# Kernel tuning notes

Measured on AMD Instinct MI355X. Metric: run time of the kernel, lower is better.

The kernel has to match this reference:

```python
import jax, jax.numpy as jnp
import numpy as np
import math

B, N, T, D, H, NOUT = 32, 20, 100, 4, 128, 16
E = N * (N - 1)
EPS = 1e-5

def _conv1d(x, w, b):
    # x: [M, Cin, L], w: [Cout, Cin, K] -> [M, Cout, L-K+1] (VALID, stride 1)
    y = jax.lax.conv_general_dilated(x, w, (1,), 'VALID', dimension_numbers=('NCH', 'OIH', 'NCH'))
    return y + b[None, :, None]

def _bn(x, g, b, axes, caxis):
    # training-mode batch norm (biased variance), eps as in torch
    m = jnp.mean(x, axis=axes, keepdims=True)
    v = jnp.var(x, axis=axes, keepdims=True)
    sh = [1] * x.ndim
    sh[caxis] = -1
    return (x - m) / jnp.sqrt(v + EPS) * g.reshape(sh) + b.reshape(sh)

def _mlp(x, w1, b1, w2, b2, g, bb):
    h = jax.nn.elu(x @ w1.T + b1)
    h = jax.nn.elu(h @ w2.T + b2)
    return _bn(h, g, bb, (0, 1), 2)  # BN over B*E samples per feature

def _forward(rel_rec, rel_send, inputs, conv1_w, conv1_b, bn1_g, bn1_b, conv2_w, conv2_b, bn2_g, bn2_b, pred_w, pred_b, att_w, att_b, mlp1_w1, mlp1_b1, mlp1_w2, mlp1_b2, mlp1_g, mlp1_bb, mlp2_w1, mlp2_b1, mlp2_w2, mlp2_b2, mlp2_g, mlp2_bb, mlp3_w1, mlp3_b1, mlp3_w2, mlp3_b2, mlp3_g, mlp3_bb, fc_out_w, fc_out_b):
    Bv, Nv, Tv, Dv = inputs.shape
    Ev = Nv * (Nv - 1)
    # node2edge_temporal: gather sender/receiver trajectories -> [B*E, 2D, T]
    xf = inputs.reshape(Bv, Nv, Tv * Dv)
    recv = jnp.einsum('en,bnf->bef', rel_rec, xf).reshape(Bv * Ev, Tv, Dv).transpose(0, 2, 1)
    send = jnp.einsum('en,bnf->bef', rel_send, xf).reshape(Bv * Ev, Tv, Dv).transpose(0, 2, 1)
    edges = jnp.concatenate([send, recv], axis=1)
    # CNN over time
    h = jax.nn.relu(_conv1d(edges, conv1_w, conv1_b))
    h = _bn(h, bn1_g, bn1_b, (0, 2), 1)
    L = h.shape[-1] // 2
    h = h[:, :, : 2 * L].reshape(h.shape[0], h.shape[1], L, 2).max(axis=-1)  # maxpool k=2 s=2
    h = jax.nn.relu(_conv1d(h, conv2_w, conv2_b))
    h = _bn(h, bn2_g, bn2_b, (0, 2), 1)
    pred = jnp.einsum('bct,oc->bot', h, pred_w[:, :, 0]) + pred_b[None, :, None]
    att = jax.nn.softmax(jnp.einsum('bct,oc->bot', h, att_w[:, :, 0]) + att_b[None, :, None], axis=-1)
    x = (pred * att).mean(axis=-1).reshape(Bv, Ev, -1)  # attention-weighted mean pool
    x = _mlp(x, mlp1_w1, mlp1_b1, mlp1_w2, mlp1_b2, mlp1_g, mlp1_bb)
    x_skip = x
    # edge2node: scatter-mean into receivers (divide by N)
    xn = jnp.einsum('en,beh->bnh', rel_rec, x) / Nv
    xn = _mlp(xn, mlp2_w1, mlp2_b1, mlp2_w2, mlp2_b2, mlp2_g, mlp2_bb)
    # node2edge: gather back to edges
    es = jnp.einsum('en,bnh->beh', rel_send, xn)
    er = jnp.einsum('en,bnh->beh', rel_rec, xn)
    x = jnp.concatenate([es, er, x_skip], axis=2)
    x = _mlp(x, mlp3_w1, mlp3_b1, mlp3_w2, mlp3_b2, mlp3_g, mlp3_bb)
    return x @ fc_out_w.T + fc_out_b

def setup_inputs() -> dict:
    key = jax.random.key(0)
    ks = iter(jax.random.split(key, 64))
    def rn(shape, scale):
        return jax.random.normal(next(ks), shape, dtype=jnp.float32) * scale
    def xav(fo, fi):
        return rn((fo, fi), math.sqrt(2.0 / (fo + fi)))
    inputs = rn((B, N, T, D), 1.0)
    pairs = np.array([(i, j) for i in range(N) for j in range(N) if i != j])
    eye = np.eye(N, dtype=np.float32)
    d = {'inputs': inputs,
         'rel_rec': jnp.asarray(eye[pairs[:, 0]]),
         'rel_send': jnp.asarray(eye[pairs[:, 1]])}
    d['conv1_w'] = rn((H, 2 * D, 5), math.sqrt(2.0 / (5 * H)))
    d['conv1_b'] = jnp.full((H,), 0.1, jnp.float32)
    d['bn1_g'] = jnp.ones((H,), jnp.float32); d['bn1_b'] = jnp.zeros((H,), jnp.float32)
    d['conv2_w'] = rn((H, H, 5), math.sqrt(2.0 / (5 * H)))
    d['conv2_b'] = jnp.full((H,), 0.1, jnp.float32)
    d['bn2_g'] = jnp.ones((H,), jnp.float32); d['bn2_b'] = jnp.zeros((H,), jnp.float32)
    d['pred_w'] = rn((H, H, 1), math.sqrt(2.0 / H))
    d['pred_b'] = jnp.full((H,), 0.1, jnp.float32)
    d['att_w'] = rn((1, H, 1), math.sqrt(2.0))
    d['att_b'] = jnp.full((1,), 0.1, jnp.float32)
    for nm, fi in (('mlp1', H), ('mlp2', H), ('mlp3', 3 * H)):
        d[nm + '_w1'] = xav(H, fi); d[nm + '_b1'] = jnp.full((H,), 0.1, jnp.float32)
        d[nm + '_w2'] = xav(H, H); d[nm + '_b2'] = jnp.full((H,), 0.1, jnp.float32)
        d[nm + '_g'] = jnp.ones((H,), jnp.float32); d[nm + '_bb'] = jnp.zeros((H,), jnp.float32)
    d['fc_out_w'] = xav(NOUT, H)
    d['fc_out_b'] = jnp.full((NOUT,), 0.1, jnp.float32)
    return d

def reference(inputs, rel_rec, rel_send, conv1_w, conv1_b, bn1_g, bn1_b, conv2_w, conv2_b, bn2_g, bn2_b, pred_w, pred_b, att_w, att_b, mlp1_w1, mlp1_b1, mlp1_w2, mlp1_b2, mlp1_g, mlp1_bb, mlp2_w1, mlp2_b1, mlp2_w2, mlp2_b2, mlp2_g, mlp2_bb, mlp3_w1, mlp3_b1, mlp3_w2, mlp3_b2, mlp3_g, mlp3_bb, fc_out_w, fc_out_b):
    return _forward(rel_rec, rel_send, inputs, conv1_w, conv1_b, bn1_g, bn1_b, conv2_w, conv2_b, bn2_g, bn2_b, pred_w, pred_b, att_w, att_b, mlp1_w1, mlp1_b1, mlp1_w2, mlp1_b2, mlp1_g, mlp1_bb, mlp2_w1, mlp2_b1, mlp2_w2, mlp2_b2, mlp2_g, mlp2_bb, mlp3_w1, mlp3_b1, mlp3_w2, mlp3_b2, mlp3_g, mlp3_bb, fc_out_w, fc_out_b)
```

## Files before the change

### kernel.cpp

```cpp
#include <hip/hip_runtime.h>
#include <hip/hip_bf16.h>
#include <hip/hip_fp16.h>

#define BB 32
#define NN 20
#define TT 100
#define DD 4
#define HH 128
#define EE 380
#define BE 12160
#define L1 96
#define LP 48
#define L2 44
#define NOUT 16
#define EPS 1e-5f
#define NREP 64

typedef _Float16 f16x8 __attribute__((ext_vector_type(8)));
typedef _Float16 f16x4 __attribute__((ext_vector_type(4)));
typedef _Float16 f16x2 __attribute__((ext_vector_type(2)));
typedef float f32x4 __attribute__((ext_vector_type(4)));

#define S_BIAS2 0
#define S_BN1_SC 256
#define S_BN2_SC 768

#define OFF_STATS 0ULL
#define OFF_SIDX 16384ULL
#define OFF_RIDX 18432ULL
#define OFF_INC 20480ULL
#define OFF_Y23 24576ULL
#define OFF_X 149446656ULL
#define OFF_BUFA 155672576ULL
#define OFF_BUFB 161898496ULL
#define OFF_XN 168124416ULL
#define OFF_T640 168452096ULL
#define OFF_REPM 168779776ULL
#define OFF_MP 171958272ULL
#define OFF_APACK OFF_T640
#define OFF_APACK1 (OFF_T640 + 163840ULL)
#define OFF_PWT (OFF_T640 + 180224ULL)
#define OFF_W2SUM (OFF_T640 + 245760ULL)
#define OFF_REP1 OFF_BUFA
#define OFF_REP2 (OFF_BUFA + 65536ULL)
#define MP_M1W1 0
#define MP_M1W2 16384
#define MP_M2W1 32768
#define MP_M2W2 49152
#define MP_M3W2 65536
#define MP_M3W1 81920

__device__ __forceinline__ float eluf(float v) { return v > 0.f ? v : expm1f(v); }

__global__ __launch_bounds__(256) void k_prep(const float* __restrict__ rel_rec,
                                              const float* __restrict__ rel_send,
                                              const float* __restrict__ w2,
                                              const float* __restrict__ w1,
                                              const float* __restrict__ pred_w,
                                              const float* __restrict__ m1w1,
                                              const float* __restrict__ m1w2,
                                              const float* __restrict__ m2w1,
                                              const float* __restrict__ m2w2,
                                              const float* __restrict__ m3w1,
                                              const float* __restrict__ m3w2,
                                              _Float16* __restrict__ apack,
                                              _Float16* __restrict__ apack1,
                                              float* __restrict__ pwt,
                                              float* __restrict__ w2sum,
                                              _Float16* __restrict__ mp,
                                              float* rep1, float* rep2, float* repm,
                                              int* sidx, int* ridx, int* inc) {
    int b = blockIdx.x;
    int tid = threadIdx.x;
    int l = tid & 63;
    if (b < 40) {
        int f = b * 4 + (tid >> 6);
        int m0 = f & 7, ks = f >> 3, s = ks & 3, k = ks >> 2;
        int m = m0 * 16 + (l & 15);
        int cbase = 32 * s + (l >> 4) * 8;
#pragma unroll
        for (int j = 0; j < 8; ++j)
            apack[(f * 64 + l) * 8 + j] = (_Float16)w2[m * 640 + (cbase + j) * 5 + k];
    } else if (b < 44) {
        int f = (b - 40) * 4 + (tid >> 6);
        int m0 = f & 7, s = f >> 3;
        int m = m0 * 16 + (l & 15);
        int cbase = 32 * s + (l >> 4) * 8;
#pragma unroll
        for (int j = 0; j < 8; ++j) {
            int c = cbase + j;
            int k = c >> 3, ci = c & 7;
            apack1[(f * 64 + l) * 8 + j] = (k < 5) ? (_Float16)w1[m * 40 + ci * 5 + k]
                                                   : (_Float16)0.f;
        }
    } else if (b == 44) {
        for (int i = tid; i < NREP * 256; i += 256) { rep1[i] = 0.f; rep2[i] = 0.f; }
        for (int i = tid; i < 3 * NREP * 256; i += 256) repm[i] = 0.f;
        for (int e = tid; e < EE; e += 256) {
            int s = 0, r = 0;
            for (int n = 0; n < NN; ++n) {
                if (rel_send[e * NN + n] > 0.5f) s = n;
                if (rel_rec[e * NN + n] > 0.5f) r = n;
            }
            sidx[e] = s; ridx[e] = r;
        }
        __syncthreads();
        if (tid < NN) {
            int k = 0;
// ... 91 lines not shown
                    s_y2t[(t >> 1) * 136 + co0 + r] = (_Float16)fmaxf(v, p);
            }
        }
#pragma unroll
        for (int r = 0; r < 4; ++r) {
            float s = ss[r], q = qq[r];
            s += __shfl_xor(s, 1); s += __shfl_xor(s, 2); s += __shfl_xor(s, 4); s += __shfl_xor(s, 8);
            q += __shfl_xor(q, 1); q += __shfl_xor(q, 2); q += __shfl_xor(q, 4); q += __shfl_xor(q, 8);
            if (l15 == 0) {
                atomicAdd(&rep[co0 + r], s);
                atomicAdd(&rep[128 + co0 + r], q);
            }
        }
    }
    __syncthreads();
    _Float16* dst = y2p + (long long)be * 6144;
    for (int chunk = threadIdx.x; chunk < 768; chunk += 256) {
        int row = chunk >> 4, off = (chunk & 15) * 8;
        *(f16x8*)(dst + row * 128 + off) = *(const f16x8*)(&s_y2t[row * 136 + off]);
    }
}

__global__ void k_finalize_rep(float* __restrict__ rep, float* stats, int scIdx,
                               const float* __restrict__ g, const float* __restrict__ bb,
                               float inv_count) {
    int j = threadIdx.x;
    float s = 0.f, q = 0.f;
    for (int i = 0; i < NREP; ++i) {
        s += rep[i * 256 + j];
        q += rep[i * 256 + 128 + j];
    }
    for (int i = 0; i < NREP; ++i) {
        rep[i * 256 + j] = 0.f;
        rep[i * 256 + 128 + j] = 0.f;
    }
    float m = s * inv_count;
    float v = fmaxf(q * inv_count - m * m, 0.f);
    float sc = g[j] * rsqrtf(v + EPS);
    stats[scIdx + j] = sc;
    stats[scIdx + 128 + j] = bb[j] - m * sc;
}

__global__ void k_finalize_bn1(float* __restrict__ rep, float* stats,
                               const float* __restrict__ g, const float* __restrict__ bb,
                               const float* __restrict__ w2sum, const float* __restrict__ conv2_b,
                               float inv_count) {
    __shared__ float s_sh[128];
    int j = threadIdx.x;
    float s = 0.f, q = 0.f;
    for (int i = 0; i < NREP; ++i) {
        s += rep[i * 256 + j];
        q += rep[i * 256 + 128 + j];
    }
    for (int i = 0; i < NREP; ++i) {
        rep[i * 256 + j] = 0.f;
        rep[i * 256 + 128 + j] = 0.f;
    }
    float m = s * inv_count;
    float v = fmaxf(q * inv_count - m * m, 0.f);
    float sc = g[j] * rsqrtf(v + EPS);
    float sh = bb[j] - m * sc;
    stats[S_BN1_SC + j] = sc;
    stats[S_BN1_SC + 128 + j] = sh;
    s_sh[j] = sh;
    __syncthreads();
    float acc = conv2_b[j];
    for (int ci = 0; ci < 128; ++ci)
        acc = fmaf(w2sum[j * 128 + ci], s_sh[ci], acc);
    stats[S_BIAS2 + j] = acc;
}

__global__ __launch_bounds__(256) void k_scale(_Float16* __restrict__ apack,
                                               const float* __restrict__ stats) {
    int tid = threadIdx.x, l = tid & 63;
    int f = blockIdx.x * 4 + (tid >> 6);
    int s = (f >> 3) & 3;
    int cbase = 32 * s + (l >> 4) * 8;
    _Float16* p = apack + (f * 64 + l) * 8;
#pragma unroll
    for (int j = 0; j < 8; ++j)
        p[j] = (_Float16)((float)p[j] * stats[S_BN1_SC + cbase + j]);
}

__global__ __launch_bounds__(256) void k_conv2(_Float16* __restrict__ y23,
                                               const _Float16* __restrict__ apack,
                                               const float* __restrict__ stats,
                                               float* rep2) {
    __shared__ __align__(16) _Float16 s_y2t[2][48 * 136];
    int tid = threadIdx.x;
    int be0 = blockIdx.x * 2;
    for (int i = tid; i < 1536; i += 256) {
        int ed = i / 768, rem = i - ed * 768;
        int row = rem >> 4, c0 = (rem & 15) * 8;
        *(f16x8*)(&s_y2t[ed][row * 136 + c0]) =
            *(const f16x8*)(y23 + (long long)(be0 + ed) * 6144 + rem * 8);
    }
    __syncthreads();
    int w = tid >> 6, lane = tid & 63;
    int quad = lane >> 4, l15 = lane & 15;
    int g = w & 1, e = w >> 1;
    f32x4 acc[4][3];
#pragma unroll
    for (int m = 0; m < 4; ++m)
#pragma unroll
        for (int nt = 0; nt < 3; ++nt) acc[m][nt] = (f32x4){0.f, 0.f, 0.f, 0.f};
    const f16x8* Ap = (const f16x8*)apack;
    const char* base = (const char*)&s_y2t[e][0];
#pragma unroll
    for (int k = 0; k < 5; ++k) {
#pragma unroll
        for (int s = 0; s < 4; ++s) {
            f16x8 am[4];
#pragma unroll
            for (int m = 0; m < 4; ++m)
                am[m] = Ap[((k * 4 + s) * 8 + g * 4 + m) * 64 + lane];
#pragma unroll
            for (int nt = 0; nt < 3; ++nt) {
                int r = nt * 16 + l15 + k;
                if (nt == 2) r = (r > 47) ? 47 : r;
                f16x8 bfr = *(const f16x8*)(base + r * 272 + 64 * s + quad * 16);
#pragma unroll
                for (int m = 0; m < 4; ++m)
                    acc[m][nt] = __builtin_amdgcn_mfma_f32_16x16x32_f16(am[m], bfr, acc[m][nt], 0, 0, 0);
            }
        }
    }
    int be = be0 + e;
    _Float16* y3 = y23 + (long long)be * 6144;
    float* rep = rep2 + (be & (NREP - 1)) * 256;
#pragma unroll
    for (int m = 0; m < 4; ++m) {
        int co0 = (g * 4 + m) * 16 + quad * 4;
        float4 bs = *(const float4*)(stats + S_BIAS2 + co0);
        float ssum[4] = {0.f, 0.f, 0.f, 0.f}, qsum[4] = {0.f, 0.f, 0.f, 0.f};
#pragma unroll
        for (int nt = 0; nt < 3; ++nt) {
            int t = nt * 16 + l15;
            if (t < 44) {
                float v0 = fmaxf(acc[m][nt][0] + bs.x, 0.f);
                float v1 = fmaxf(acc[m][nt][1] + bs.y, 0.f);
                float v2 = fmaxf(acc[m][nt][2] + bs.z, 0.f);
                float v3 = fmaxf(acc[m][nt][3] + bs.w, 0.f);
                f16x4 o = {(_Float16)v0, (_Float16)v1, (_Float16)v2, (_Float16)v3};
                *(f16x4*)(y3 + t * 128 + co0) = o;
                ssum[0] += v0; qsum[0] += v0 * v0;
                ssum[1] += v1; qsum[1] += v1 * v1;
                ssum[2] += v2; qsum[2] += v2 * v2;
                ssum[3] += v3; qsum[3] += v3 * v3;
            }
        }
#pragma unroll
        for (int r = 0; r < 4; ++r) {
            float s = ssum[r], q = qsum[r];
            s += __shfl_xor(s, 1); s += __shfl_xor(s, 2); s += __shfl_xor(s, 4); s += __shfl_xor(s, 8);
            q += __shfl_xor(q, 1); q += __shfl_xor(q, 2); q += __shfl_xor(q, 4); q += __shfl_xor(q, 8);
            if (l15 == 0) {
                atomicAdd(&rep[co0 + r], s);
                atomicAdd(&rep[128 + co0 + r], q);
            }
        }
    }
}

__global__ __launch_bounds__(256) void k_predatt(const _Float16* __restrict__ y23,
                                                 const float* __restrict__ stats,
                                                 const float* __restrict__ att_w,
                                                 const float* __restrict__ att_b,
                                                 const float* __restrict__ pwt,
                                                 const float* __restrict__ pred_b,
                                                 float* __restrict__ x) {
    __shared__ float h[44 * 132];
    __shared__ float s_att[48];
    __shared__ float s_p1[256];
    __shared__ float s_p2[256];
    __shared__ float s_sc[128], s_sh[128];
    int be = blockIdx.x, tid = threadIdx.x;
    if (tid < 128) {
        s_sc[tid] = stats[S_BN2_SC + tid];
        s_sh[tid] = stats[S_BN2_SC + 128 + tid];
    }
    __syncthreads();
    const _Float16* yp = y23 + (long long)be * 6144;
    for (int i = tid; i < 704; i += 256) {
        int t = i >> 4, c0 = (i & 15) * 8;
        f16x8 v = *(const f16x8*)(yp + i * 8);
        float4 a, bq;
        a.x = fmaf((float)v[0], s_sc[c0 + 0], s_sh[c0 + 0]);
        a.y = fmaf((float)v[1], s_sc[c0 + 1], s_sh[c0 + 1]);
        a.z = fmaf((float)v[2], s_sc[c0 + 2], s_sh[c0 + 2]);
        a.w = fmaf((float)v[3], s_sc[c0 + 3], s_sh[c0 + 3]);
        bq.x = fmaf((float)v[4], s_sc[c0 + 4], s_sh[c0 + 4]);
        bq.y = fmaf((float)v[5], s_sc[c0 + 5], s_sh[c0 + 5]);
        bq.z = fmaf((float)v[6], s_sc[c0 + 6], s_sh[c0 + 6]);
        bq.w = fmaf((float)v[7], s_sc[c0 + 7], s_sh[c0 + 7]);
        *(float4*)(&h[t * 132 + c0]) = a;
        *(float4*)(&h[t * 132 + c0 + 4]) = bq;
    }
    __syncthreads();
    int w = tid >> 6, lane = tid & 63;
    {
        float aw0 = att_w[lane], aw1 = att_w[64 + lane];
        for (int tt = 0; tt < 11; ++tt) {
            int t = w * 11 + tt;
            float p = h[t * 132 + lane] * aw0 + h[t * 132 + 64 + lane] * aw1;
            p += __shfl_xor(p, 1); p += __shfl_xor(p, 2); p += __shfl_xor(p, 4);
            p += __shfl_xor(p, 8); p += __shfl_xor(p, 16); p += __shfl_xor(p, 32);
            if (lane == 0) s_att[t] = p + att_b[0];
        }
    }
    __syncthreads();
    if (w == 0) {
        float v = (lane < 44) ? s_att[lane] : -1e30f;
        float m = v;
        m = fmaxf(m, __shfl_xor(m, 1)); m = fmaxf(m, __shfl_xor(m, 2));
        m = fmaxf(m, __shfl_xor(m, 4)); m = fmaxf(m, __shfl_xor(m, 8));
        m = fmaxf(m, __shfl_xor(m, 16)); m = fmaxf(m, __shfl_xor(m, 32));
        float ev = (lane < 44) ? expf(v - m) : 0.f;
        float ss = ev;
        ss += __shfl_xor(ss, 1); ss += __shfl_xor(ss, 2); ss += __shfl_xor(ss, 4);
        ss += __shfl_xor(ss, 8); ss += __shfl_xor(ss, 16); ss += __shfl_xor(ss, 32);
        if (lane < 44) s_att[lane] = ev / ss;
    }
    __syncthreads();
    {
        int c = tid & 127, hh = tid >> 7;
        float a = 0.f;
        for (int t = hh * 22; t < hh * 22 + 22; ++t) a = fmaf(h[t * 132 + c], s_att[t], a);
        s_p1[tid] = a;
    }
    __syncthreads();
    {
        int o = tid & 127, hh = tid >> 7;
        float a = 0.f;
        for (int c = hh * 64; c < hh * 64 + 64; ++c) {
            float hw = s_p1[c] + s_p1[128 + c];
            a = fmaf(pwt[c * 128 + o], hw, a);
        }
        s_p2[tid] = a;
    }
    __syncthreads();
    if (tid < 128) {
        float a = s_p2[tid] + s_p2[128 + tid] + pred_b[tid];
        x[(long long)be * 128 + tid] = a * (1.0f / 44.0f);
    }
}

__global__ __launch_bounds__(256) void k_mlp2x(const float* __restrict__ in,
                                               const _Float16* __restrict__ wp1,
                                               const float* __restrict__ b1,
                                               const _Float16* __restrict__ wp2,
                                               const float* __restrict__ b2,
                                               float* __restrict__ out,
                                               float* __restrict__ repm) {
    __shared__ __align__(16) _Float16 s_in[64 * 136];
    __shared__ __align__(16) _Float16 s_mid[64 * 136];
    int tid = threadIdx.x;
    long long r0 = (long long)blockIdx.x * 64;
    {
        const float4* src = (const float4*)(in + r0 * 128);
        for (int i = tid; i < 2048; i += 256) {
            int row = i >> 5, c0 = (i & 31) * 4;
            float4 v = src[i];
            f16x4 o = {(_Float16)v.x, (_Float16)v.y, (_Float16)v.z, (_Float16)v.w};
            *(f16x4*)(&s_in[row * 136 + c0]) = o;
        }
    }
    __syncthreads();
    int w = tid >> 6, lane = tid & 63, quad = lane >> 4, l15 = lane & 15;
    {
        f32x4 acc[2][4];
#pragma unroll
        for (int m = 0; m < 2; ++m)
#pragma unroll
            for (int nt = 0; nt < 4; ++nt) acc[m][nt] = (f32x4){0.f, 0.f, 0.f, 0.f};
        const f16x8* Ap = (const f16x8*)wp1;
#pragma unroll
        for (int s = 0; s < 4; ++s) {
            f16x8 a0 = Ap[(s * 8 + 2 * w) * 64 + lane];
            f16x8 a1 = Ap[(s * 8 + 2 * w + 1) * 64 + lane];
#pragma unroll
            for (int nt = 0; nt < 4; ++nt) {
                f16x8 bfr = *(const f16x8*)((const char*)s_in + (nt * 16 + l15) * 272 + 64 * s + quad * 16);
                acc[0][nt] = __builtin_amdgcn_mfma_f32_16x16x32_f16(a0, bfr, acc[0][nt], 0, 0, 0);
                acc[1][nt] = __builtin_amdgcn_mfma_f32_16x16x32_f16(a1, bfr, acc[1][nt], 0, 0, 0);
            }
        }
#pragma unroll
        for (int m = 0; m < 2; ++m) {
            int j0 = (2 * w + m) * 16 + quad * 4;
            float4 bs = *(const float4*)(b1 + j0);
#pragma unroll
            for (int nt = 0; nt < 4; ++nt) {
                int row = nt * 16 + l15;
                f16x4 o = {(_Float16)eluf(acc[m][nt][0] + bs.x),
                           (_Float16)eluf(acc[m][nt][1] + bs.y),
                           (_Float16)eluf(acc[m][nt][2] + bs.z),
                           (_Float16)eluf(acc[m][nt][3] + bs.w)};
                *(f16x4*)(&s_mid[row * 136 + j0]) = o;
            }
        }
    }
    __syncthreads();
    {
        f32x4 acc[2][4];
#pragma unroll
        for (int m = 0; m < 2; ++m)
#pragma unroll
            for (int nt = 0; nt < 4; ++nt) acc[m][nt] = (f32x4){0.f, 0.f, 0.f, 0.f};
        const f16x8* Ap = (const f16x8*)wp2;
#pragma unroll
        for (int s = 0; s < 4; ++s) {
            f16x8 a0 = Ap[(s * 8 + 2 * w) * 64 + lane];
            f16x8 a1 = Ap[(s * 8 + 2 * w + 1) * 64 + lane];
#pragma unroll
            for (int nt = 0; nt < 4; ++nt) {
                f16x8 bfr = *(const f16x8*)((const char*)s_mid + (nt * 16 + l15) * 272 + 64 * s + quad * 16);
                acc[0][nt] = __builtin_amdgcn_mfma_f32_16x16x32_f16(a0, bfr, acc[0][nt], 0, 0, 0);
                acc[1][nt] = __builtin_amdgcn_mfma_f32_16x16x32_f16(a1, bfr, acc[1][nt], 0, 0, 0);
            }
        }
#pragma unroll
        for (int m = 0; m < 2; ++m) {
            int j0 = (2 * w + m) * 16 + quad * 4;
            float4 bs = *(const float4*)(b2 + j0);
            float ss[4] = {0.f, 0.f, 0.f, 0.f}, qq[4] = {0.f, 0.f, 0.f, 0.f};
#pragma unroll
// ... 207 lines not shown
    __shared__ float s_w[16 * 129];
    __shared__ float s_sc[128], s_sh[128];
    int r0 = blockIdx.x * 16;
    int tid = threadIdx.x;
    if (tid < 128) {
        float s = 0.f, q = 0.f;
        for (int i = 0; i < NREP; ++i) {
            s += repm3[i * 256 + tid];
            q += repm3[i * 256 + 128 + tid];
        }
        float mm = s * (1.0f / (float)BE);
        float vv = fmaxf(q * (1.0f / (float)BE) - mm * mm, 0.f);
        float sc = m3g[tid] * rsqrtf(vv + EPS);
        s_sc[tid] = sc;
        s_sh[tid] = m3bb[tid] - mm * sc;
    }
    __syncthreads();
    for (int i = tid; i < 16 * 128; i += 256) {
        int rr = i >> 7, j = i & 127;
        s_x[rr * 129 + j] = fmaf(h2[(long long)(r0 + rr) * 128 + j], s_sc[j], s_sh[j]);
    }
    for (int i = tid; i < 16 * 128; i += 256) {
        int o = i >> 7, j = i & 127;
        s_w[o * 129 + j] = fcw[i];
    }
    __syncthreads();
    int rl = tid >> 4, o = tid & 15;
    float a = fcb[o];
    for (int j = 0; j < 128; ++j) a = fmaf(s_x[rl * 129 + j], s_w[o * 129 + j], a);
    out[(long long)(r0 + rl) * 16 + o] = a;
}

extern "C" void kernel_launch(void* const* d_in, const int* in_sizes, int n_in,
                              void* d_out, int out_size, void* d_ws, size_t ws_size,
                              hipStream_t stream) {
    const float* inputs = (const float*)d_in[0];
    const float* rel_rec = (const float*)d_in[1];
    const float* rel_send = (const float*)d_in[2];
    const float* conv1_w = (const float*)d_in[3];
    const float* conv1_b = (const float*)d_in[4];
    const float* bn1_g = (const float*)d_in[5];
    const float* bn1_b = (const float*)d_in[6];
    const float* conv2_w = (const float*)d_in[7];
    const float* conv2_b = (const float*)d_in[8];
    const float* bn2_g = (const float*)d_in[9];
    const float* bn2_b = (const float*)d_in[10];
    const float* pred_w = (const float*)d_in[11];
    const float* pred_b = (const float*)d_in[12];
    const float* att_w = (const float*)d_in[13];
    const float* att_b = (const float*)d_in[14];
    const float* m1w1 = (const float*)d_in[15];
    const float* m1b1 = (const float*)d_in[16];
    const float* m1w2 = (const float*)d_in[17];
    const float* m1b2 = (const float*)d_in[18];
    const float* m1g = (const float*)d_in[19];
    const float* m1bb = (const float*)d_in[20];
    const float* m2w1 = (const float*)d_in[21];
    const float* m2b1 = (const float*)d_in[22];
    const float* m2w2 = (const float*)d_in[23];
    const float* m2b2 = (const float*)d_in[24];
    const float* m2g = (const float*)d_in[25];
    const float* m2bb = (const float*)d_in[26];
    const float* m3w1 = (const float*)d_in[27];
    const float* m3b1 = (const float*)d_in[28];
    const float* m3w2 = (const float*)d_in[29];
    const float* m3b2 = (const float*)d_in[30];
    const float* m3g = (const float*)d_in[31];
    const float* m3bb = (const float*)d_in[32];
    const float* fcw = (const float*)d_in[33];
    const float* fcb = (const float*)d_in[34];

    char* ws = (char*)d_ws;
    float* stats = (float*)(ws + OFF_STATS);
    int* sidx = (int*)(ws + OFF_SIDX);
    int* ridx = (int*)(ws + OFF_RIDX);
    int* inc = (int*)(ws + OFF_INC);
    _Float16* y23 = (_Float16*)(ws + OFF_Y23);
    float* x = (float*)(ws + OFF_X);
    float* bufB = (float*)(ws + OFF_BUFB);
    float* xn = (float*)(ws + OFF_XN);
    _Float16* apack = (_Float16*)(ws + OFF_APACK);
    _Float16* apack1 = (_Float16*)(ws + OFF_APACK1);
    float* pwt = (float*)(ws + OFF_PWT);
    float* w2sum = (float*)(ws + OFF_W2SUM);
    float* rep1 = (float*)(ws + OFF_REP1);
    float* rep2 = (float*)(ws + OFF_REP2);
    float* repm1 = (float*)(ws + OFF_REPM);
    float* repm2 = (float*)(ws + OFF_REPM + 65536ULL);
    float* repm3 = (float*)(ws + OFF_REPM + 131072ULL);
    _Float16* mp = (_Float16*)(ws + OFF_MP);
    float* outp = (float*)d_out;

    hipLaunchKernelGGL(k_prep, dim3(125), dim3(256), 0, stream,
                       rel_rec, rel_send, conv2_w, conv1_w, pred_w,
                       m1w1, m1w2, m2w1, m2w2, m3w1, m3w2,
                       apack, apack1, pwt, w2sum, mp, rep1, rep2, repm1, sidx, ridx, inc);
    hipLaunchKernelGGL(k_conv1_stats, dim3(BE), dim3(256), 0, stream,
                       inputs, apack1, conv1_b, sidx, ridx, rep1, y23);
    hipLaunchKernelGGL(k_finalize_bn1, dim3(1), dim3(128), 0, stream,
                       rep1, stats, bn1_g, bn1_b, w2sum, conv2_b, 1.0f / (float)(BE * L1));
    hipLaunchKernelGGL(k_scale, dim3(40), dim3(256), 0, stream, apack, stats);
    hipLaunchKernelGGL(k_conv2, dim3(BE / 2), dim3(256), 0, stream,
                       y23, apack, stats, rep2);
    hipLaunchKernelGGL(k_finalize_rep, dim3(1), dim3(128), 0, stream,
                       rep2, stats, S_BN2_SC, bn2_g, bn2_b, 1.0f / (float)(BE * L2));
    hipLaunchKernelGGL(k_predatt, dim3(BE), dim3(256), 0, stream,
                       y23, stats, att_w, att_b, pwt, pred_b, x);
    hipLaunchKernelGGL(k_mlp2x, dim3(BE / 64), dim3(256), 0, stream,
                       x, mp + MP_M1W1, m1b1, mp + MP_M1W2, m1b2, bufB, repm1);
    hipLaunchKernelGGL(k_e2n, dim3(BB * NN), dim3(128), 0, stream, bufB, inc, repm1, m1g, m1bb, xn);
    hipLaunchKernelGGL(k_mlp2x, dim3(BB * NN / 64), dim3(256), 0, stream,
                       xn, mp + MP_M2W1, m2b1, mp + MP_M2W2, m2b2, xn, repm2);
    hipLaunchKernelGGL(k_mlp3x, dim3(BE / 64), dim3(256), 0, stream,
                       xn, bufB, sidx, ridx, repm1, repm2, m1g, m1bb, m2g, m2bb,
                       mp + MP_M3W1, m3b1, mp + MP_M3W2, m3b2, bufB, repm3);
    hipLaunchKernelGGL(k_fcout, dim3(BE / 16), dim3(256), 0, stream,
                       bufB, repm3, m3g, m3bb, fcw, fcb, outp);
    (void)in_sizes; (void)n_in; (void)out_size; (void)ws_size;
}
```

Baseline: 587.0 us.

## Process four edges per conv2 block with A-fragment reuse and staged coalesced stores

The conv2 kernel now handles four edge sequences per block, and each wave computes two edges so every loaded weight fragment feeds twice as many MFMAs. Weight fragments are double-buffered across the K/S loop to overlap their global loads with compute. Outputs are written into shared memory first and then copied out with coalesced 16-byte stores instead of scattered 8-byte stores. The cost is double the accumulator registers (launch_bounds with 2 blocks/SM), double the shared memory, and half as many blocks.

```diff
diff --git a/kernel.cpp b/kernel.cpp
--- a/kernel.cpp
+++ b/kernel.cpp
@@ -281,84 +281,124 @@
         p[j] = (_Float16)((float)p[j] * stats[S_BN1_SC + cbase + j]);
 }
 
-__global__ __launch_bounds__(256) void k_conv2(_Float16* __restrict__ y23,
-                                               const _Float16* __restrict__ apack,
-                                               const float* __restrict__ stats,
-                                               float* rep2) {
-    __shared__ __align__(16) _Float16 s_y2t[2][48 * 136];
+#define C2_COMPUTE(AM, K, S)                                                          \
+    do {                                                                              \
+        int rbase = ((K) * 272) + ((S) * 64) + lquad16 + l15x272;                     \
+        _Pragma("unroll")                                                             \
+        for (int nt = 0; nt < 3; ++nt) {                                              \
+            int ro = rbase + nt * (16 * 272);                                         \
+            if (nt == 2) { int rr = 32 + l15 + (K); if (rr > 47) ro -= (rr - 47) * 272; } \
+            f16x8 b0 = *(const f16x8*)(baseE0 + ro);                                  \
+            f16x8 b1 = *(const f16x8*)(baseE1 + ro);                                  \
+            _Pragma("unroll")                                                         \
+            for (int m = 0; m < 4; ++m) {                                             \
+                acc0[m][nt] = __builtin_amdgcn_mfma_f32_16x16x32_f16(AM[m], b0, acc0[m][nt], 0, 0, 0); \
+                acc1[m][nt] = __builtin_amdgcn_mfma_f32_16x16x32_f16(AM[m], b1, acc1[m][nt], 0, 0, 0); \
+            }                                                                         \
+        }                                                                             \
+    } while (0)
+
+#define C2_EPILOG(ACC, EE)                                                            \
+    do {                                                                              \
+        int e_loc = ep * 2 + (EE);                                                    \
+        long long bee = be0 + e_loc;                                                  \
+        float* rep = rep2 + ((int)(bee & (NREP - 1))) * 256;                          \
+        _Float16* sout = &s_y2t[e_loc][0];                                            \
+        _Pragma("unroll")                                                             \
+        for (int m = 0; m < 4; ++m) {                                                 \
+            int co0 = (g * 4 + m) * 16 + quad * 4;                                    \
+            float4 bs = *(const float4*)(stats + S_BIAS2 + co0);                      \
+            float ssum[4] = {0.f, 0.f, 0.f, 0.f}, qsum[4] = {0.f, 0.f, 0.f, 0.f};     \
+            _Pragma("unroll")                                                         \
+            for (int nt = 0; nt < 3; ++nt) {                                          \
+                int t = nt * 16 + l15;                                                \
+                if (t < 44) {                                                         \
+                    float v0 = fmaxf(ACC[m][nt][0] + bs.x, 0.f);                      \
+                    float v1 = fmaxf(ACC[m][nt][1] + bs.y, 0.f);                      \
+                    float v2 = fmaxf(ACC[m][nt][2] + bs.z, 0.f);                      \
+                    float v3 = fmaxf(ACC[m][nt][3] + bs.w, 0.f);                      \
+                    f16x4 o = {(_Float16)v0, (_Float16)v1, (_Float16)v2, (_Float16)v3}; \
+                    *(f16x4*)(sout + t * 136 + co0) = o;                              \
+                    ssum[0] += v0; qsum[0] += v0 * v0;                                \
+                    ssum[1] += v1; qsum[1] += v1 * v1;                                \
+                    ssum[2] += v2; qsum[2] += v2 * v2;                                \
+                    ssum[3] += v3; qsum[3] += v3 * v3;                                \
+                }                                                                     \
+            }                                                                         \
+            _Pragma("unroll")                                                         \
+            for (int r = 0; r < 4; ++r) {                                             \
+                float s = ssum[r], q = qsum[r];                                       \
+                s += __shfl_xor(s, 1); s += __shfl_xor(s, 2); s += __shfl_xor(s, 4); s += __shfl_xor(s, 8); \
+                q += __shfl_xor(q, 1); q += __shfl_xor(q, 2); q += __shfl_xor(q, 4); q += __shfl_xor(q, 8); \
+                if (l15 == 0) {                                                       \
+                    atomicAdd(&rep[co0 + r], s);                                      \
+                    atomicAdd(&rep[128 + co0 + r], q);                                \
+                }                                                                     \
+            }                                                                         \
+        }                                                                             \
+    } while (0)
+
+__global__ __launch_bounds__(256, 2) void k_conv2(_Float16* __restrict__ y23,
+                                                  const _Float16* __restrict__ apack,
+                                                  const float* __restrict__ stats,
+                                                  float* rep2) {
+    __shared__ __align__(16) _Float16 s_y2t[4][48 * 136];
     int tid = threadIdx.x;
-    int be0 = blockIdx.x * 2;
-    for (int i = tid; i < 1536; i += 256) {
-        int ed = i / 768, rem = i - ed * 768;
-        int row = rem >> 4, c0 = (rem & 15) * 8;
-        *(f16x8*)(&s_y2t[ed][row * 136 + c0]) =
-            *(const f16x8*)(y23 + (long long)(be0 + ed) * 6144 + rem * 8);
-    }
+    long long be0 = (long long)blockIdx.x * 4;
+#pragma unroll
+    for (int ed = 0; ed < 4; ++ed)
+        for (int rem = tid; rem < 768; rem += 256) {
+            int row = rem >> 4, c0 = (rem & 15) * 8;
+            *(f16x8*)(&s_y2t[ed][row * 136 + c0]) =
+                *(const f16x8*)(y23 + (be0 + ed) * 6144 + rem * 8);
+        }
     __syncthreads();
     int w = tid >> 6, lane = tid & 63;
     int quad = lane >> 4, l15 = lane & 15;
-    int g = w & 1, e = w >> 1;
-    f32x4 acc[4][3];
+    int g = w & 1, ep = w >> 1;
+    int lquad16 = quad * 16;
+    int l15x272 = l15 * 272;
+    const char* baseE0 = (const char*)&s_y2t[ep * 2][0];
+    const char* baseE1 = (const char*)&s_y2t[ep * 2 + 1][0];
+    f32x4 acc0[4][3], acc1[4][3];
 #pragma unroll
     for (int m = 0; m < 4; ++m)
 #pragma unroll
-        for (int nt = 0; nt < 3; ++nt) acc[m][nt] = (f32x4){0.f, 0.f, 0.f, 0.f};
+        for (int nt = 0; nt < 3; ++nt) {
+            acc0[m][nt] = (f32x4){0.f, 0.f, 0.f, 0.f};
+            acc1[m][nt] = (f32x4){0.f, 0.f, 0.f, 0.f};
+        }
     const f16x8* Ap = (const f16x8*)apack;
-    const char* base = (const char*)&s_y2t[e][0];
-#pragma unroll
-    for (int k = 0; k < 5; ++k) {
-#pragma unroll
-        for (int s = 0; s < 4; ++s) {
-            f16x8 am[4];
-#pragma unroll
-            for (int m = 0; m < 4; ++m)
-                am[m] = Ap[((k * 4 + s) * 8 + g * 4 + m) * 64 + lane];
-#pragma unroll
-            for (int nt = 0; nt < 3; ++nt) {
-                int r = nt * 16 + l15 + k;
-                if (nt == 2) r = (r > 47) ? 47 : r;
-                f16x8 bfr = *(const f16x8*)(base + r * 272 + 64 * s + quad * 16);
-#pragma unroll
-                for (int m = 0; m < 4; ++m)
-                    acc[m][nt] = __builtin_amdgcn_mfma_f32_16x16x32_f16(am[m], bfr, acc[m][nt], 0, 0, 0);
-            }
-        }
-    }
-    int be = be0 + e;
-    _Float16* y3 = y23 + (long long)be * 6144;
-    float* rep = rep2 + (be & (NREP - 1)) * 256;
-#pragma unroll
-    for (int m = 0; m < 4; ++m) {
-        int co0 = (g * 4 + m) * 16 + quad * 4;
-        float4 bs = *(const float4*)(stats + S_BIAS2 + co0);
-        float ssum[4] = {0.f, 0.f, 0.f, 0.f}, qsum[4] = {0.f, 0.f, 0.f, 0.f};
-#pragma unroll
-        for (int nt = 0; nt < 3; ++nt) {
-            int t = nt * 16 + l15;
-            if (t < 44) {
-                float v0 = fmaxf(acc[m][nt][0] + bs.x, 0.f);
-                float v1 = fmaxf(acc[m][nt][1] + bs.y, 0.f);
-                float v2 = fmaxf(acc[m][nt][2] + bs.z, 0.f);
-                float v3 = fmaxf(acc[m][nt][3] + bs.w, 0.f);
-                f16x4 o = {(_Float16)v0, (_Float16)v1, (_Float16)v2, (_Float16)v3};
-                *(f16x4*)(y3 + t * 128 + co0) = o;
-                ssum[0] += v0; qsum[0] += v0 * v0;
-                ssum[1] += v1; qsum[1] += v1 * v1;
-                ssum[2] += v2; qsum[2] += v2 * v2;
-                ssum[3] += v3; qsum[3] += v3 * v3;
-            }
-        }
-#pragma unroll
-        for (int r = 0; r < 4; ++r) {
-            float s = ssum[r], q = qsum[r];
-            s += __shfl_xor(s, 1); s += __shfl_xor(s, 2); s += __shfl_xor(s, 4); s += __shfl_xor(s, 8);
-            q += __shfl_xor(q, 1); q += __shfl_xor(q, 2); q += __shfl_xor(q, 4); q += __shfl_xor(q, 8);
-            if (l15 == 0) {
-                atomicAdd(&rep[co0 + r], s);
-                atomicAdd(&rep[128 + co0 + r], q);
-            }
-        }
-    }
+    f16x8 amA[4], amB[4];
+#pragma unroll
+    for (int m = 0; m < 4; ++m) amA[m] = Ap[(g * 4 + m) * 64 + lane];
+    for (int it = 0; it < 20; it += 2) {
+#pragma unroll
+        for (int m = 0; m < 4; ++m) amB[m] = Ap[((it + 1) * 8 + g * 4 + m) * 64 + lane];
+        {
+            int k = it >> 2, s = it & 3;
+            C2_COMPUTE(amA, k, s);
+        }
+        if (it + 2 < 20) {
+#pragma unroll
+            for (int m = 0; m < 4; ++m) amA[m] = Ap[((it + 2) * 8 + g * 4 + m) * 64 + lane];
+        }
+        {
+            int k = (it + 1) >> 2, s = (it + 1) & 3;
+            C2_COMPUTE(amB, k, s);
+        }
+    }
+    __syncthreads();
+    C2_EPILOG(acc0, 0);
+    C2_EPILOG(acc1, 1);
+    __syncthreads();
+#pragma unroll
+    for (int ed = 0; ed < 4; ++ed)
+        for (int rem = tid; rem < 704; rem += 256) {
+            int row = rem >> 4, c0 = (rem & 15) * 8;
+            *(f16x8*)(y23 + (be0 + ed) * 6144 + rem * 8) =
+                *(const f16x8*)(&s_y2t[ed][row * 136 + c0]);
+        }
 }
 
 __global__ __launch_bounds__(256) void k_predatt(const _Float16* __restrict__ y23,
@@ -832,7 +872,7 @@
     hipLaunchKernelGGL(k_finalize_bn1, dim3(1), dim3(128), 0, stream,
                        rep1, stats, bn1_g, bn1_b, w2sum, conv2_b, 1.0f / (float)(BE * L1));
     hipLaunchKernelGGL(k_scale, dim3(40), dim3(256), 0, stream, apack, stats);
-    hipLaunchKernelGGL(k_conv2, dim3(BE / 2), dim3(256), 0, stream,
+    hipLaunchKernelGGL(k_conv2, dim3(BE / 4), dim3(256), 0, stream,
                        y23, apack, stats, rep2);
     hipLaunchKernelGGL(k_finalize_rep, dim3(1), dim3(128), 0, stream,
                        rep2, stats, S_BN2_SC, bn2_g, bn2_b, 1.0f / (float)(BE * L2));
```

Result: slower. 606.8 us (+3.4%).

## Split conv2 across 8 waves with two output tiles each and double-buffered A loads

Applied to the files above, without the earlier changes.

The conv2 kernel goes from 256 to 512 threads per block, so each wave computes 2 instead of 4 output-channel tiles. This cuts accumulator registers per wave and raises occupancy, with launch bounds allowing 6 blocks. The A-fragment loads are software-pipelined with two register buffers so the next k-step's weights load while the current MFMAs run. The cost is that each B fragment read from LDS now feeds only 2 MFMAs instead of 4, so LDS read traffic per MFMA roughly doubles.

```diff
diff --git a/kernel.cpp b/kernel.cpp
--- a/kernel.cpp
+++ b/kernel.cpp
@@ -281,55 +281,63 @@
         p[j] = (_Float16)((float)p[j] * stats[S_BN1_SC + cbase + j]);
 }
 
-__global__ __launch_bounds__(256) void k_conv2(_Float16* __restrict__ y23,
-                                               const _Float16* __restrict__ apack,
-                                               const float* __restrict__ stats,
-                                               float* rep2) {
+__global__ __launch_bounds__(512, 6) void k_conv2(_Float16* __restrict__ y23,
+                                                  const _Float16* __restrict__ apack,
+                                                  const float* __restrict__ stats,
+                                                  float* rep2) {
     __shared__ __align__(16) _Float16 s_y2t[2][48 * 136];
     int tid = threadIdx.x;
-    int be0 = blockIdx.x * 2;
-    for (int i = tid; i < 1536; i += 256) {
+    long long be0 = (long long)blockIdx.x * 2;
+    for (int i = tid; i < 1536; i += 512) {
         int ed = i / 768, rem = i - ed * 768;
-        int row = rem >> 4, c0 = (rem & 15) * 8;
-        *(f16x8*)(&s_y2t[ed][row * 136 + c0]) =
-            *(const f16x8*)(y23 + (long long)(be0 + ed) * 6144 + rem * 8);
+        *(f16x8*)(&s_y2t[ed][(rem >> 4) * 136 + (rem & 15) * 8]) =
+            *(const f16x8*)(y23 + (be0 + ed) * 6144 + rem * 8);
     }
     __syncthreads();
     int w = tid >> 6, lane = tid & 63;
     int quad = lane >> 4, l15 = lane & 15;
-    int g = w & 1, e = w >> 1;
-    f32x4 acc[4][3];
-#pragma unroll
-    for (int m = 0; m < 4; ++m)
+    int g2 = w & 3, ep = w >> 2;
+    const char* base = (const char*)&s_y2t[ep][0];
+    int rb0 = quad * 16 + l15 * 272;
+    f32x4 acc[2][3];
+#pragma unroll
+    for (int m = 0; m < 2; ++m)
 #pragma unroll
         for (int nt = 0; nt < 3; ++nt) acc[m][nt] = (f32x4){0.f, 0.f, 0.f, 0.f};
     const f16x8* Ap = (const f16x8*)apack;
-    const char* base = (const char*)&s_y2t[e][0];
-#pragma unroll
-    for (int k = 0; k < 5; ++k) {
-#pragma unroll
-        for (int s = 0; s < 4; ++s) {
-            f16x8 am[4];
-#pragma unroll
-            for (int m = 0; m < 4; ++m)
-                am[m] = Ap[((k * 4 + s) * 8 + g * 4 + m) * 64 + lane];
-#pragma unroll
-            for (int nt = 0; nt < 3; ++nt) {
-                int r = nt * 16 + l15 + k;
-                if (nt == 2) r = (r > 47) ? 47 : r;
-                f16x8 bfr = *(const f16x8*)(base + r * 272 + 64 * s + quad * 16);
-#pragma unroll
-                for (int m = 0; m < 4; ++m)
-                    acc[m][nt] = __builtin_amdgcn_mfma_f32_16x16x32_f16(am[m], bfr, acc[m][nt], 0, 0, 0);
-            }
-        }
-    }
-    int be = be0 + e;
-    _Float16* y3 = y23 + (long long)be * 6144;
-    float* rep = rep2 + (be & (NREP - 1)) * 256;
-#pragma unroll
-    for (int m = 0; m < 4; ++m) {
-        int co0 = (g * 4 + m) * 16 + quad * 4;
+    f16x8 amA[2], amB[2];
+#pragma unroll
+    for (int m = 0; m < 2; ++m) amA[m] = Ap[(g2 * 2 + m) * 64 + lane];
+#define C2_STEP(AM, IT)                                                               \
+    do {                                                                              \
+        int k = (IT) >> 2, s = (IT) & 3;                                              \
+        int rbase = k * 272 + s * 64 + rb0;                                           \
+        _Pragma("unroll")                                                             \
+        for (int nt = 0; nt < 3; ++nt) {                                              \
+            int ro = rbase + nt * (16 * 272);                                         \
+            if (nt == 2) { int rr = 32 + l15 + k; if (rr > 47) ro -= (rr - 47) * 272; } \
+            f16x8 bfr = *(const f16x8*)(base + ro);                                   \
+            acc[0][nt] = __builtin_amdgcn_mfma_f32_16x16x32_f16(AM[0], bfr, acc[0][nt], 0, 0, 0); \
+            acc[1][nt] = __builtin_amdgcn_mfma_f32_16x16x32_f16(AM[1], bfr, acc[1][nt], 0, 0, 0); \
+        }                                                                             \
+    } while (0)
+    for (int it = 0; it < 20; it += 2) {
+#pragma unroll
+        for (int m = 0; m < 2; ++m) amB[m] = Ap[((it + 1) * 8 + g2 * 2 + m) * 64 + lane];
+        C2_STEP(amA, it);
+        if (it + 2 < 20) {
+#pragma unroll
+            for (int m = 0; m < 2; ++m) amA[m] = Ap[((it + 2) * 8 + g2 * 2 + m) * 64 + lane];
+        }
+        C2_STEP(amB, it + 1);
+    }
+#undef C2_STEP
+    long long be = be0 + ep;
+    _Float16* y3 = y23 + be * 6144;
+    float* rep = rep2 + ((int)(be & (NREP - 1))) * 256;
+#pragma unroll
+    for (int m = 0; m < 2; ++m) {
+        int co0 = (g2 * 2 + m) * 16 + quad * 4;
         float4 bs = *(const float4*)(stats + S_BIAS2 + co0);
         float ssum[4] = {0.f, 0.f, 0.f, 0.f}, qsum[4] = {0.f, 0.f, 0.f, 0.f};
 #pragma unroll
@@ -832,7 +840,7 @@
     hipLaunchKernelGGL(k_finalize_bn1, dim3(1), dim3(128), 0, stream,
                        rep1, stats, bn1_g, bn1_b, w2sum, conv2_b, 1.0f / (float)(BE * L1));
     hipLaunchKernelGGL(k_scale, dim3(40), dim3(256), 0, stream, apack, stats);
-    hipLaunchKernelGGL(k_conv2, dim3(BE / 2), dim3(256), 0, stream,
+    hipLaunchKernelGGL(k_conv2, dim3(BE / 2), dim3(512), 0, stream,
                        y23, apack, stats, rep2);
     hipLaunchKernelGGL(k_finalize_rep, dim3(1), dim3(128), 0, stream,
                        rep2, stats, S_BN2_SC, bn2_g, bn2_b, 1.0f / (float)(BE * L2));
```

New measurement: 594.7 us. Within noise of the previous version (+1.3%).

## Fold BN2 affine into pred/att weights and move pred projection into MFMA MLP

Applied to the files above, without the earlier changes.

Folds the BN2 scale into the attention weights and the pred weight matrix, and the BN2 shift into the pred bias, in a new small prep kernel. The attention bias is dropped because softmax is shift-invariant. k_predatt now keeps the raw fp16 activations in LDS and outputs only the attention-pooled 128-vector, skipping the per-edge scalar 128x128 pred matvec. That projection runs as an extra MFMA GEMM stage at the front of a fused three-layer MLP kernel. This removes per-block scalar FMA work and halves LDS use, at the cost of fp16 rounding of the folded pred weights and the intermediate result.

```diff
diff --git a/kernel.cpp b/kernel.cpp
--- a/kernel.cpp
+++ b/kernel.cpp
@@ -24,6 +24,8 @@
 #define S_BIAS2 0
 #define S_BN1_SC 256
 #define S_BN2_SC 768
+#define S_AW2 1280
+#define S_PB2 1536
 
 #define OFF_STATS 0ULL
 #define OFF_SIDX 16384ULL
@@ -361,50 +363,55 @@
     }
 }
 
+__global__ __launch_bounds__(256) void k_predpack(float* __restrict__ stats,
+                                                  const float* __restrict__ pred_w,
+                                                  const float* __restrict__ pred_b,
+                                                  const float* __restrict__ att_w,
+                                                  _Float16* __restrict__ mpred) {
+    int b = blockIdx.x, tid = threadIdx.x, l = tid & 63;
+    if (b < 8) {
+        int f = b * 4 + (tid >> 6);
+        int m = (f & 7) * 16 + (l & 15);
+        int cb = 32 * (f >> 3) + (l >> 4) * 8;
+#pragma unroll
+        for (int j = 0; j < 8; ++j) {
+            int c = cb + j;
+            mpred[(f * 64 + l) * 8 + j] =
+                (_Float16)(pred_w[m * 128 + c] * stats[S_BN2_SC + c] * (1.0f / 44.0f));
+        }
+    } else if (tid < 128) {
+        float a = pred_b[tid];
+        for (int c = 0; c < 128; ++c)
+            a = fmaf(pred_w[tid * 128 + c], stats[S_BN2_SC + 128 + c], a);
+        stats[S_PB2 + tid] = a * (1.0f / 44.0f);
+        stats[S_AW2 + tid] = stats[S_BN2_SC + tid] * att_w[tid];
+    }
+}
+
 __global__ __launch_bounds__(256) void k_predatt(const _Float16* __restrict__ y23,
                                                  const float* __restrict__ stats,
-                                                 const float* __restrict__ att_w,
-                                                 const float* __restrict__ att_b,
-                                                 const float* __restrict__ pwt,
-                                                 const float* __restrict__ pred_b,
                                                  float* __restrict__ x) {
-    __shared__ float h[44 * 132];
+    __shared__ __align__(16) _Float16 s_y3[44 * 136];
     __shared__ float s_att[48];
     __shared__ float s_p1[256];
-    __shared__ float s_p2[256];
-    __shared__ float s_sc[128], s_sh[128];
+    __shared__ float s_aw[128];
     int be = blockIdx.x, tid = threadIdx.x;
-    if (tid < 128) {
-        s_sc[tid] = stats[S_BN2_SC + tid];
-        s_sh[tid] = stats[S_BN2_SC + 128 + tid];
-    }
-    __syncthreads();
+    if (tid < 128) s_aw[tid] = stats[S_AW2 + tid];
     const _Float16* yp = y23 + (long long)be * 6144;
     for (int i = tid; i < 704; i += 256) {
         int t = i >> 4, c0 = (i & 15) * 8;
-        f16x8 v = *(const f16x8*)(yp + i * 8);
-        float4 a, bq;
-        a.x = fmaf((float)v[0], s_sc[c0 + 0], s_sh[c0 + 0]);
-        a.y = fmaf((float)v[1], s_sc[c0 + 1], s_sh[c0 + 1]);
-        a.z = fmaf((float)v[2], s_sc[c0 + 2], s_sh[c0 + 2]);
-        a.w = fmaf((float)v[3], s_sc[c0 + 3], s_sh[c0 + 3]);
-        bq.x = fmaf((float)v[4], s_sc[c0 + 4], s_sh[c0 + 4]);
-        bq.y = fmaf((float)v[5], s_sc[c0 + 5], s_sh[c0 + 5]);
-        bq.z = fmaf((float)v[6], s_sc[c0 + 6], s_sh[c0 + 6]);
-        bq.w = fmaf((float)v[7], s_sc[c0 + 7], s_sh[c0 + 7]);
-        *(float4*)(&h[t * 132 + c0]) = a;
-        *(float4*)(&h[t * 132 + c0 + 4]) = bq;
+        *(f16x8*)(&s_y3[t * 136 + c0]) = *(const f16x8*)(yp + i * 8);
     }
     __syncthreads();
     int w = tid >> 6, lane = tid & 63;
     {
-        float aw0 = att_w[lane], aw1 = att_w[64 + lane];
+        float aw0 = s_aw[lane], aw1 = s_aw[64 + lane];
         for (int tt = 0; tt < 11; ++tt) {
             int t = w * 11 + tt;
-            float p = h[t * 132 + lane] * aw0 + h[t * 132 + 64 + lane] * aw1;
+            float p = (float)s_y3[t * 136 + lane] * aw0 + (float)s_y3[t * 136 + 64 + lane] * aw1;
             p += __shfl_xor(p, 1); p += __shfl_xor(p, 2); p += __shfl_xor(p, 4);
             p += __shfl_xor(p, 8); p += __shfl_xor(p, 16); p += __shfl_xor(p, 32);
-            if (lane == 0) s_att[t] = p + att_b[0];
+            if (lane == 0) s_att[t] = p;
         }
     }
     __syncthreads();
@@ -424,23 +431,156 @@
     {
         int c = tid & 127, hh = tid >> 7;
         float a = 0.f;
-        for (int t = hh * 22; t < hh * 22 + 22; ++t) a = fmaf(h[t * 132 + c], s_att[t], a);
+        for (int t = hh * 22; t < hh * 22 + 22; ++t)
+            a = fmaf((float)s_y3[t * 136 + c], s_att[t], a);
         s_p1[tid] = a;
     }
     __syncthreads();
-    {
-        int o = tid & 127, hh = tid >> 7;
-        float a = 0.f;
-        for (int c = hh * 64; c < hh * 64 + 64; ++c) {
-            float hw = s_p1[c] + s_p1[128 + c];
-            a = fmaf(pwt[c * 128 + o], hw, a);
-        }
-        s_p2[tid] = a;
-    }
-    __syncthreads();
-    if (tid < 128) {
-        float a = s_p2[tid] + s_p2[128 + tid] + pred_b[tid];
-        x[(long long)be * 128 + tid] = a * (1.0f / 44.0f);
+    if (tid < 128)
+        x[(long long)be * 128 + tid] = s_p1[tid] + s_p1[128 + tid];
+}
+
+__global__ __launch_bounds__(256) void k_mlp1x(const float* __restrict__ in,
+                                               const _Float16* __restrict__ wp0,
+                                               const float* __restrict__ stats,
+                                               const _Float16* __restrict__ wp1,
+                                               const float* __restrict__ b1,
+                                               const _Float16* __restrict__ wp2,
+                                               const float* __restrict__ b2,
+                                               float* __restrict__ out,
+                                               float* __restrict__ repm) {
+    __shared__ __align__(16) _Float16 s_a[64 * 136];
+    __shared__ __align__(16) _Float16 s_b[64 * 136];
+    int tid = threadIdx.x;
+    long long r0 = (long long)blockIdx.x * 64;
+    {
+        const float4* src = (const float4*)(in + r0 * 128);
+        for (int i = tid; i < 2048; i += 256) {
+            int row = i >> 5, c0 = (i & 31) * 4;
+            float4 v = src[i];
+            f16x4 o = {(_Float16)v.x, (_Float16)v.y, (_Float16)v.z, (_Float16)v.w};
+            *(f16x4*)(&s_a[row * 136 + c0]) = o;
+        }
+    }
+    __syncthreads();
+    int w = tid >> 6, lane = tid & 63, quad = lane >> 4, l15 = lane & 15;
+    {
+        f32x4 acc[2][4];
+#pragma unroll
+        for (int m = 0; m < 2; ++m)
+#pragma unroll
+            for (int nt = 0; nt < 4; ++nt) acc[m][nt] = (f32x4){0.f, 0.f, 0.f, 0.f};
+        const f16x8* Ap = (const f16x8*)wp0;
+#pragma unroll
+        for (int s = 0; s < 4; ++s) {
+            f16x8 a0 = Ap[(s * 8 + 2 * w) * 64 + lane];
+            f16x8 a1 = Ap[(s * 8 + 2 * w + 1) * 64 + lane];
+#pragma unroll
+            for (int nt = 0; nt < 4; ++nt) {
+                f16x8 bfr = *(const f16x8*)((const char*)s_a + (nt * 16 + l15) * 272 + 64 * s + quad * 16);
+                acc[0][nt] = __builtin_amdgcn_mfma_f32_16x16x32_f16(a0, bfr, acc[0][nt], 0, 0, 0);
+                acc[1][nt] = __builtin_amdgcn_mfma_f32_16x16x32_f16(a1, bfr, acc[1][nt], 0, 0, 0);
+            }
+        }
+#pragma unroll
+        for (int m = 0; m < 2; ++m) {
+            int j0 = (2 * w + m) * 16 + quad * 4;
+            float4 bs = *(const float4*)(stats + S_PB2 + j0);
+#pragma unroll
+            for (int nt = 0; nt < 4; ++nt) {
+                int row = nt * 16 + l15;
+                f16x4 o = {(_Float16)(acc[m][nt][0] + bs.x),
+                           (_Float16)(acc[m][nt][1] + bs.y),
+                           (_Float16)(acc[m][nt][2] + bs.z),
+                           (_Float16)(acc[m][nt][3] + bs.w)};
+                *(f16x4*)(&s_b[row * 136 + j0]) = o;
+            }
+        }
+    }
+    __syncthreads();
+    {
+        f32x4 acc[2][4];
+#pragma unroll
+        for (int m = 0; m < 2; ++m)
+#pragma unroll
+            for (int nt = 0; nt < 4; ++nt) acc[m][nt] = (f32x4){0.f, 0.f, 0.f, 0.f};
+        const f16x8* Ap = (const f16x8*)wp1;
+#pragma unroll
+        for (int s = 0; s < 4; ++s) {
+            f16x8 a0 = Ap[(s * 8 + 2 * w) * 64 + lane];
+            f16x8 a1 = Ap[(s * 8 + 2 * w + 1) * 64 + lane];
+#pragma unroll
+            for (int nt = 0; nt < 4; ++nt) {
+                f16x8 bfr = *(const f16x8*)((const char*)s_b + (nt * 16 + l15) * 272 + 64 * s + quad * 16);
+                acc[0][nt] = __builtin_amdgcn_mfma_f32_16x16x32_f16(a0, bfr, acc[0][nt], 0, 0, 0);
+                acc[1][nt] = __builtin_amdgcn_mfma_f32_16x16x32_f16(a1, bfr, acc[1][nt], 0, 0, 0);
+            }
+        }
+#pragma unroll
+        for (int m = 0; m < 2; ++m) {
+            int j0 = (2 * w + m) * 16 + quad * 4;
+            float4 bs = *(const float4*)(b1 + j0);
+#pragma unroll
+            for (int nt = 0; nt < 4; ++nt) {
+                int row = nt * 16 + l15;
+                f16x4 o = {(_Float16)eluf(acc[m][nt][0] + bs.x),
+                           (_Float16)eluf(acc[m][nt][1] + bs.y),
+                           (_Float16)eluf(acc[m][nt][2] + bs.z),
+                           (_Float16)eluf(acc[m][nt][3] + bs.w)};
+                *(f16x4*)(&s_a[row * 136 + j0]) = o;
+            }
+        }
+    }
+    __syncthreads();
+    {
+        f32x4 acc[2][4];
+#pragma unroll
+        for (int m = 0; m < 2; ++m)
+#pragma unroll
+            for (int nt = 0; nt < 4; ++nt) acc[m][nt] = (f32x4){0.f, 0.f, 0.f, 0.f};
+        const f16x8* Ap = (const f16x8*)wp2;
+#pragma unroll
+        for (int s = 0; s < 4; ++s) {
+            f16x8 a0 = Ap[(s * 8 + 2 * w) * 64 + lane];
+            f16x8 a1 = Ap[(s * 8 + 2 * w + 1) * 64 + lane];
+#pragma unroll
+            for (int nt = 0; nt < 4; ++nt) {
+                f16x8 bfr = *(const f16x8*)((const char*)s_a + (nt * 16 + l15) * 272 + 64 * s + quad * 16);
+                acc[0][nt] = __builtin_amdgcn_mfma_f32_16x16x32_f16(a0, bfr, acc[0][nt], 0, 0, 0);
+                acc[1][nt] = __builtin_amdgcn_mfma_f32_16x16x32_f16(a1, bfr, acc[1][nt], 0, 0, 0);
+            }
+        }
+#pragma unroll
+        for (int m = 0; m < 2; ++m) {
+            int j0 = (2 * w + m) * 16 + quad * 4;
+            float4 bs = *(const float4*)(b2 + j0);
+            float ss[4] = {0.f, 0.f, 0.f, 0.f}, qq[4] = {0.f, 0.f, 0.f, 0.f};
+#pragma unroll
+            for (int nt = 0; nt < 4; ++nt) {
+                int row = nt * 16 + l15;
+                float v0 = eluf(acc[m][nt][0] + bs.x);
+                float v1 = eluf(acc[m][nt][1] + bs.y);
+                float v2 = eluf(acc[m][nt][2] + bs.z);
+                float v3 = eluf(acc[m][nt][3] + bs.w);
+                float4 o = {v0, v1, v2, v3};
+                *(float4*)(out + (r0 + row) * 128 + j0) = o;
+                ss[0] += v0; qq[0] += v0 * v0;
+                ss[1] += v1; qq[1] += v1 * v1;
+                ss[2] += v2; qq[2] += v2 * v2;
+                ss[3] += v3; qq[3] += v3 * v3;
+            }
+            float* rep = repm + (blockIdx.x & (NREP - 1)) * 256;
+#pragma unroll
+            for (int r = 0; r < 4; ++r) {
+                float s = ss[r], q = qq[r];
+                s += __shfl_xor(s, 1); s += __shfl_xor(s, 2); s += __shfl_xor(s, 4); s += __shfl_xor(s, 8);
+                q += __shfl_xor(q, 1); q += __shfl_xor(q, 2); q += __shfl_xor(q, 4); q += __shfl_xor(q, 8);
+                if (l15 == 0) {
+                    atomicAdd(&rep[j0 + r], s);
+                    atomicAdd(&rep[128 + j0 + r], q);
+                }
+            }
+        }
     }
 }
 
@@ -814,6 +954,7 @@
     _Float16* apack = (_Float16*)(ws + OFF_APACK);
     _Float16* apack1 = (_Float16*)(ws + OFF_APACK1);
     float* pwt = (float*)(ws + OFF_PWT);
+    _Float16* mpred = (_Float16*)(ws + OFF_PWT);
     float* w2sum = (float*)(ws + OFF_W2SUM);
     float* rep1 = (float*)(ws + OFF_REP1);
     float* rep2 = (float*)(ws + OFF_REP2);
@@ -836,10 +977,11 @@
                        y23, apack, stats, rep2);
     hipLaunchKernelGGL(k_finalize_rep, dim3(1), dim3(128), 0, stream,
                        rep2, stats, S_BN2_SC, bn2_g, bn2_b, 1.0f / (float)(BE * L2));
-    hipLaunchKernelGGL(k_predatt, dim3(BE), dim3(256), 0, stream,
-                       y23, stats, att_w, att_b, pwt, pred_b, x);
-    hipLaunchKernelGGL(k_mlp2x, dim3(BE / 64), dim3(256), 0, stream,
-                       x, mp + MP_M1W1, m1b1, mp + MP_M1W2, m1b2, bufB, repm1);
+    hipLaunchKernelGGL(k_predpack, dim3(9), dim3(256), 0, stream,
+                       stats, pred_w, pred_b, att_w, mpred);
+    hipLaunchKernelGGL(k_predatt, dim3(BE), dim3(256), 0, stream, y23, stats, x);
+    hipLaunchKernelGGL(k_mlp1x, dim3(BE / 64), dim3(256), 0, stream,
+                       x, mpred, stats, mp + MP_M1W1, m1b1, mp + MP_M1W2, m1b2, bufB, repm1);
     hipLaunchKernelGGL(k_e2n, dim3(BB * NN), dim3(128), 0, stream, bufB, inc, repm1, m1g, m1bb, xn);
     hipLaunchKernelGGL(k_mlp2x, dim3(BB * NN / 64), dim3(256), 0, stream,
                        xn, mp + MP_M2W1, m2b1, mp + MP_M2W2, m2b2, xn, repm2);
@@ -849,4 +991,5 @@
     hipLaunchKernelGGL(k_fcout, dim3(BE / 16), dim3(256), 0, stream,
                        bufB, repm3, m3g, m3bb, fcw, fcb, outp);
     (void)in_sizes; (void)n_in; (void)out_size; (void)ws_size;
-}
+    (void)att_b;
+}
```

New measurement: 619.8 us. +5.6%, slower.
